# Kernel optimization log

Hardware: AMD Instinct MI355X
Metric: run time of the kernel (lower is better)

The kernel has to match this reference:

```python
import jax, jax.numpy as jnp
import numpy as np


def setup_inputs() -> dict:
    key = jax.random.key(0)
    k1, k2 = jax.random.split(key)
    _input = jax.random.normal(k1, (64, 8, 256, 256), dtype=jnp.float32)
    _filter = jax.random.normal(k2, (8, 8, 3, 3), dtype=jnp.float32)
    return {"_input": _input, "_filter": _filter}


def reference(_input, _filter):
    # The original module builds an im2col buffer with Python loops and does a
    # single GEMM; the math is exactly a stride-1, VALID-padding cross-correlation:
    #   out[n,m,i,j] = sum_{c,r,s} input[n,c,i+r,j+s] * filter[m,c,r,s]
    # Expressed as the efficient implicit-GEMM convolution primitive.
    out = jax.lax.conv_general_dilated(
        _input, _filter,
        window_strides=(1, 1),
        padding="VALID",
        dimension_numbers=("NCHW", "OIHW", "NCHW"),
    )
    return out  # (N, M, H-R+1, W-S+1)
```

## Files before the change

kernel.cpp:

```cpp
#include <hip/hip_runtime.h>


typedef _Float16 half8 __attribute__((ext_vector_type(8)));
typedef float floatx4 __attribute__((ext_vector_type(4)));

#define SLOT_H 8192

__global__ __launch_bounds__(256, 2)
void conv2d_mfma_kernel(const float* __restrict__ inp,
                        const float* __restrict__ filt,
                        float* __restrict__ out) {
    __shared__ __align__(16) _Float16 s_in[3 * SLOT_H];
    __shared__ __align__(16) float    s_out[4 * 2048];

    const int tid    = threadIdx.x;
    const int ystrip = blockIdx.x * 32;
    const int n      = blockIdx.y;

    const float* in_n  = inp + (size_t)n * (8 * 256 * 256);
    float*       out_n = out + (size_t)n * (8 * 254 * 254);

    const int lane = tid & 63;
    const int w    = tid >> 6;
    const int lx   = lane & 15;
    const int g    = lane >> 4;
    const int lx4  = tid & 63;

    half8 afrag[3];
    int   roff[3];
    int   loH[3][4];
    #pragma unroll
    for (int kk = 0; kk < 3; ++kk) {
        int q  = kk * 4 + g;
        int qa = q > 8 ? 8 : q;
        roff[kk] = qa / 3;
        int soff = qa - roff[kk] * 3;
        int q0   = lx + soff;
        int e    = (q0 & 3) ^ ((q0 >> 2) & 3);
        int q0b  = q0 >> 4;
        int baseH = (q0 >> 2) * 32;
        #pragma unroll
        for (int j = 0; j < 4; ++j)
            loH[kk][j] = baseH + ((e ^ ((j + q0b) & 3)) << 3);
        half8 a = {};
        if (q <= 8 && lx < 8) {
            #pragma unroll
            for (int j = 0; j < 8; ++j)
                a[j] = (_Float16)filt[lx * 72 + j * 9 + q];
        }
        afrag[kk] = a;
    }

    float4 vv[8];
    auto load_chunk = [&](int ck) {
        const int iy = ystrip + ck * 4 + w;
        if (iy < 256) {
            const float* p = in_n + iy * 256 + lx4 * 4;
            #pragma unroll
            for (int c = 0; c < 8; ++c)
                vv[c] = *reinterpret_cast<const float4*>(p + c * 65536);
        } else {
            #pragma unroll
            for (int c = 0; c < 8; ++c) vv[c] = make_float4(0.f,0.f,0.f,0.f);
        }
    };
    auto write_chunk = [&](int ck) {
        _Float16* base = &s_in[(ck % 3) * SLOT_H + w * 2048 + lx4 * 32];
        const int sw = (lx4 & 3) ^ ((lx4 >> 2) & 3);
        #pragma unroll
        for (int i = 0; i < 4; ++i) {
            half8 h;
            #pragma unroll
            for (int c = 0; c < 8; ++c) h[c] = (_Float16)vv[c][i];
            *reinterpret_cast<half8*>(base + ((i ^ sw) << 3)) = h;
        }
    };

    load_chunk(0); write_chunk(0);
    load_chunk(1); write_chunk(1);
    __syncthreads();

    for (int t = 0; t < 8; ++t) {
        if (t < 7) load_chunk(t + 2);
        __builtin_amdgcn_sched_barrier(0);

        const int ro = t * 4 + w;
        const int oy = ystrip + ro;

        int ab[3][4];
        #pragma unroll
        for (int kk = 0; kk < 3; ++kk) {
            int L    = ro + roff[kk];
            int rbH  = ((L >> 2) % 3) * SLOT_H + (L & 3) * 2048;
            #pragma unroll
            for (int j = 0; j < 4; ++j) ab[kk][j] = rbH + loH[kk][j];
        }

        const bool do_out = (g < 2) && (oy < 254);
        #pragma unroll
        for (int xg = 0; xg < 16; ++xg) {
            floatx4 acc = {0.f, 0.f, 0.f, 0.f};
            #pragma unroll
            for (int kk = 0; kk < 3; ++kk) {
                const half8 b = *reinterpret_cast<const half8*>(
                    &s_in[ab[kk][xg & 3] + xg * 128]);
                acc = __builtin_amdgcn_mfma_f32_16x16x32_f16(
                          afrag[kk], b, acc, 0, 0, 0);
            }
            if (do_out) {
                #pragma unroll
                for (int i = 0; i < 4; ++i)
                    s_out[w * 2048 + (g * 4 + i) * 256 + xg * 16 + lx] = acc[i];
            }
        }

        if (oy < 254) {
            #pragma unroll
            for (int m = 0; m < 8; ++m) {
                float4 q4 = *reinterpret_cast<const float4*>(
                    &s_out[w * 2048 + m * 256 + lane * 4]);
                float* op = out_n + (size_t)m * 64516 + oy * 254 + lane * 4;
                *reinterpret_cast<float2*>(op) = make_float2(q4.x, q4.y);
                if (lane < 63)
                    *reinterpret_cast<float2*>(op + 2) = make_float2(q4.z, q4.w);
            }
        }

        if (t < 7) write_chunk(t + 2);
        __syncthreads();
    }
}

extern "C" void kernel_launch(void* const* d_in, const int* in_sizes, int n_in,
                              void* d_out, int out_size, void* d_ws, size_t ws_size,
                              hipStream_t stream) {
    const float* inp  = (const float*)d_in[0];
    const float* filt = (const float*)d_in[1];
    float* outp = (float*)d_out;

    dim3 grid(8, 64, 1);
    dim3 block(256);
    conv2d_mfma_kernel<<<grid, block, 0, stream>>>(inp, filt, outp);
}
```

Before: 258.3 us.

## Halve row strip per block, double-buffer LDS, and split output staging for occupancy

Each block now processes 16 output rows instead of 32, with twice as many blocks. The input ring shrinks from triple to double buffering with an extra barrier before refilling, and output staging is split into two half-row passes so s_out is halved. Launch bounds raise the target to 3 blocks per CU. The aim is more resident blocks to hide memory latency, at the cost of more halo row re-reads per block and an extra sync per iteration.

```diff
diff --git a/kernel.cpp b/kernel.cpp
--- a/kernel.cpp
+++ b/kernel.cpp
@@ -6,15 +6,15 @@
 
 #define SLOT_H 8192
 
-__global__ __launch_bounds__(256, 2)
+__global__ __launch_bounds__(256, 3)
 void conv2d_mfma_kernel(const float* __restrict__ inp,
                         const float* __restrict__ filt,
                         float* __restrict__ out) {
-    __shared__ __align__(16) _Float16 s_in[3 * SLOT_H];
-    __shared__ __align__(16) float    s_out[4 * 2048];
+    __shared__ __align__(16) _Float16 s_in[2 * SLOT_H + 32];
+    __shared__ __align__(16) float    s_out[4 * 1024];
 
     const int tid    = threadIdx.x;
-    const int ystrip = blockIdx.x * 32;
+    const int ystrip = blockIdx.x * 16;
     const int n      = blockIdx.y;
 
     const float* in_n  = inp + (size_t)n * (8 * 256 * 256);
@@ -24,7 +24,7 @@
     const int w    = tid >> 6;
     const int lx   = lane & 15;
     const int g    = lane >> 4;
-    const int lx4  = tid & 63;
+    const int lx4  = lane;
 
     half8 afrag[3];
     int   roff[3];
@@ -51,37 +51,39 @@
         afrag[kk] = a;
     }
 
-    float4 vv[8];
-    auto load_chunk = [&](int ck) {
+    auto load_chunk = [&](int ck, float4* dst) {
         const int iy = ystrip + ck * 4 + w;
         if (iy < 256) {
             const float* p = in_n + iy * 256 + lx4 * 4;
             #pragma unroll
             for (int c = 0; c < 8; ++c)
-                vv[c] = *reinterpret_cast<const float4*>(p + c * 65536);
+                dst[c] = *reinterpret_cast<const float4*>(p + c * 65536);
         } else {
             #pragma unroll
-            for (int c = 0; c < 8; ++c) vv[c] = make_float4(0.f,0.f,0.f,0.f);
+            for (int c = 0; c < 8; ++c) dst[c] = make_float4(0.f,0.f,0.f,0.f);
         }
     };
-    auto write_chunk = [&](int ck) {
-        _Float16* base = &s_in[(ck % 3) * SLOT_H + w * 2048 + lx4 * 32];
+    auto write_chunk = [&](int ck, const float4* src) {
+        _Float16* base = &s_in[(ck & 1) * SLOT_H + w * 2048 + lx4 * 32];
         const int sw = (lx4 & 3) ^ ((lx4 >> 2) & 3);
         #pragma unroll
         for (int i = 0; i < 4; ++i) {
             half8 h;
             #pragma unroll
-            for (int c = 0; c < 8; ++c) h[c] = (_Float16)vv[c][i];
+            for (int c = 0; c < 8; ++c) h[c] = (_Float16)src[c][i];
             *reinterpret_cast<half8*>(base + ((i ^ sw) << 3)) = h;
         }
     };
 
-    load_chunk(0); write_chunk(0);
-    load_chunk(1); write_chunk(1);
+    float4 vv[8], vv2[8];
+    load_chunk(0, vv);
+    load_chunk(1, vv2);
+    write_chunk(0, vv);
+    write_chunk(1, vv2);
     __syncthreads();
 
-    for (int t = 0; t < 8; ++t) {
-        if (t < 7) load_chunk(t + 2);
+    for (int t = 0; t < 4; ++t) {
+        if (t < 3) load_chunk(t + 2, vv);
         __builtin_amdgcn_sched_barrier(0);
 
         const int ro = t * 4 + w;
@@ -90,44 +92,51 @@
         int ab[3][4];
         #pragma unroll
         for (int kk = 0; kk < 3; ++kk) {
-            int L    = ro + roff[kk];
-            int rbH  = ((L >> 2) % 3) * SLOT_H + (L & 3) * 2048;
+            int L   = ro + roff[kk];
+            int rbH = ((L >> 2) & 1) * SLOT_H + (L & 3) * 2048;
             #pragma unroll
             for (int j = 0; j < 4; ++j) ab[kk][j] = rbH + loH[kk][j];
         }
 
         const bool do_out = (g < 2) && (oy < 254);
         #pragma unroll
-        for (int xg = 0; xg < 16; ++xg) {
-            floatx4 acc = {0.f, 0.f, 0.f, 0.f};
+        for (int xh = 0; xh < 2; ++xh) {
             #pragma unroll
-            for (int kk = 0; kk < 3; ++kk) {
-                const half8 b = *reinterpret_cast<const half8*>(
-                    &s_in[ab[kk][xg & 3] + xg * 128]);
-                acc = __builtin_amdgcn_mfma_f32_16x16x32_f16(
-                          afrag[kk], b, acc, 0, 0, 0);
+            for (int xgl = 0; xgl < 8; ++xgl) {
+                const int xg = xh * 8 + xgl;
+                floatx4 acc = {0.f, 0.f, 0.f, 0.f};
+                #pragma unroll
+                for (int kk = 0; kk < 3; ++kk) {
+                    const half8 b = *reinterpret_cast<const half8*>(
+                        &s_in[ab[kk][xg & 3] + xg * 128]);
+                    acc = __builtin_amdgcn_mfma_f32_16x16x32_f16(
+                              afrag[kk], b, acc, 0, 0, 0);
+                }
+                if (do_out) {
+                    #pragma unroll
+                    for (int i = 0; i < 4; ++i)
+                        s_out[w * 1024 + (g * 4 + i) * 128 + xgl * 16 + lx]
+                            = acc[i];
+                }
             }
-            if (do_out) {
+            if (oy < 254) {
+                const int px = xh * 128 + lane * 2;
                 #pragma unroll
-                for (int i = 0; i < 4; ++i)
-                    s_out[w * 2048 + (g * 4 + i) * 256 + xg * 16 + lx] = acc[i];
+                for (int m = 0; m < 8; ++m) {
+                    float2 q2 = *reinterpret_cast<const float2*>(
+                        &s_out[w * 1024 + m * 128 + lane * 2]);
+                    if (px < 254)
+                        *reinterpret_cast<float2*>(
+                            out_n + (size_t)m * 64516 + oy * 254 + px) = q2;
+                }
             }
         }
 
-        if (oy < 254) {
-            #pragma unroll
-            for (int m = 0; m < 8; ++m) {
-                float4 q4 = *reinterpret_cast<const float4*>(
-                    &s_out[w * 2048 + m * 256 + lane * 4]);
-                float* op = out_n + (size_t)m * 64516 + oy * 254 + lane * 4;
-                *reinterpret_cast<float2*>(op) = make_float2(q4.x, q4.y);
-                if (lane < 63)
-                    *reinterpret_cast<float2*>(op + 2) = make_float2(q4.z, q4.w);
-            }
+        if (t < 3) {
+            __syncthreads();
+            write_chunk(t + 2, vv);
+            __syncthreads();
         }
-
-        if (t < 7) write_chunk(t + 2);
-        __syncthreads();
     }
 }
 
@@ -138,7 +147,7 @@
     const float* filt = (const float*)d_in[1];
     float* outp = (float*)d_out;
 
-    dim3 grid(8, 64, 1);
+    dim3 grid(16, 64, 1);
     dim3 block(256);
     conv2d_mfma_kernel<<<grid, block, 0, stream>>>(inp, filt, outp);
 }
```

Measured after the change: 259.1 us. Within noise of the previous version (+0.3%).
